# Kernel tuning notes

Hardware: AMD Instinct MI355X
Metric: run time of the kernel (lower is better)

The kernel has to match this reference:

```python
import jax, jax.numpy as jnp
import numpy as np

B, H, W = 16, 1024, 1024
EPS = 1e-7
FG_PROB = 0.1  # foreground pixel probability for synthetic gt


def setup_inputs() -> dict:
    key = jax.random.key(0)
    k1, k2 = jax.random.split(key)
    probs = jax.random.normal(k1, (B, 2, H, W), dtype=jnp.float32)
    gt = (jax.random.uniform(k2, (B, H, W)) < FG_PROB).astype(jnp.float32)
    gt_f_num = gt.sum(axis=(1, 2))  # per-sample foreground pixel count (float)
    return {"probs": probs, "gt": gt, "gt_f_num": gt_f_num, "img_h": H, "img_w": W}


def reference(probs, gt, gt_f_num, img_h, img_w):
    # foreground probability, clamped
    pc = jax.nn.softmax(probs, axis=1)[:, 1, :, :]
    pc = jnp.clip(pc, EPS, 1.0 - EPS)
    b = pc.shape[0]
    f_loss = -(gt * jnp.log(pc)).reshape(b, -1)          # [B, N]
    b_loss = -((1.0 - gt) * jnp.log(1.0 - pc)).reshape(b, -1)  # [B, N]
    n = b_loss.shape[1]

    # sort background loss descending per sample; top gt_f_num[i] entries are
    # "difficult" negatives, the rest are "simple" (equivalent to the torch
    # gather-into-zero-buffers since only sums/counts are taken afterwards)
    sorted_b = -jnp.sort(-b_loss, axis=1)                # descending, [B, N]
    k = gt_f_num.astype(jnp.int32)                       # int(gt_f_num[i])
    mask = jnp.arange(n, dtype=jnp.int32)[None, :] < k[:, None]  # [B, N]

    difficult_sum = jnp.sum(jnp.where(mask, sorted_b, 0.0), axis=1)
    simple_sum = jnp.sum(jnp.where(mask, 0.0, sorted_b), axis=1)
    difficult_num = jnp.sum(mask & (sorted_b != 0.0), axis=1).astype(jnp.float32)

    difficult_b_loss = difficult_sum / (difficult_num + 1e-16)
    simple_b_loss = simple_sum / (float(img_h * img_w) + 1e-16)
    f_loss_mean = f_loss.sum(axis=1) / (gt_f_num + 1e-16)

    return difficult_b_loss.mean() + f_loss_mean.mean() + simple_b_loss.mean()
```

## Files before the change

kernel.cpp:

```cpp
#include <hip/hip_runtime.h>
#include <math.h>

#define NB 16
#define NPIX 1048576
#define BINS 2048
#define CHUNKS 64
#define TPB_A 1024
#define PIX_PER_BLOCK (NPIX / CHUNKS)
#define QUADS 4
#define REPL 8
#define TPB_B 256
#define BINS_PER_CHUNK (BINS / TPB_B)
#define BLOSS_MAX 16.7f
#define BINW (BLOSS_MAX / (float)BINS)
#define B_CAP 16.636f
#define F_CAP 16.1181f

__device__ __forceinline__ void fadd_glb(float* p, float v) {
    __hip_atomic_fetch_add(p, v, __ATOMIC_RELAXED, __HIP_MEMORY_SCOPE_AGENT);
}

__global__ __launch_bounds__(TPB_A, 8) void pass_a(
    const float* __restrict__ probs, const float* __restrict__ gt,
    unsigned* __restrict__ g_cnt, float* __restrict__ f_sum,
    float* __restrict__ b_sum)
{
    __shared__ unsigned s_cnt[BINS];
    __shared__ float s_redf[TPB_A / 64];
    __shared__ float s_redb[TPB_A / 64];

    const int tid = threadIdx.x;
    #pragma unroll
    for (int j = 0; j < BINS / TPB_A; ++j) s_cnt[j * TPB_A + tid] = 0u;
    __syncthreads();

    const int blk = blockIdx.x;
    const int b = blk / CHUNKS;
    const int chunk = blk % CHUNKS;
    const float* p0 = probs + (size_t)b * 2 * NPIX;
    const float* p1 = p0 + NPIX;
    const float* gp = gt + (size_t)b * NPIX;
    const int base = chunk * PIX_PER_BLOCK;
    const float scale = (float)BINS / BLOSS_MAX;

    float4 A0[QUADS], A1[QUADS], G[QUADS];
    #pragma unroll
    for (int q = 0; q < QUADS; ++q) {
        const int i = base + ((q * TPB_A + tid) << 2);
        A0[q] = *(const float4*)(p0 + i);
        A1[q] = *(const float4*)(p1 + i);
        G[q]  = *(const float4*)(gp + i);
    }

    float f_acc = 0.f, b_acc = 0.f;
    #pragma unroll
    for (int q = 0; q < QUADS; ++q) {
        const float dv[4] = {A1[q].x - A0[q].x, A1[q].y - A0[q].y,
                             A1[q].z - A0[q].z, A1[q].w - A0[q].w};
        const float gv[4] = {G[q].x, G[q].y, G[q].z, G[q].w};
        #pragma unroll
        for (int c = 0; c < 4; ++c) {
            const float d = dv[c];
            const float g = gv[c];
            const float sp = fmaxf(d, 0.f) + __logf(1.f + __expf(-fabsf(d)));
            f_acc += g * fminf(sp - d, F_CAP);
            const float bl = fminf(sp, B_CAP);
            b_acc += (1.f - g) * bl;
            if (g < 0.5f) {
                int bin = (int)(bl * scale);
                bin = bin < (BINS - 1) ? bin : (BINS - 1);
                atomicAdd(&s_cnt[bin], 1u);
            }
        }
    }
    __syncthreads();

    {
        unsigned* dst = g_cnt + ((size_t)b * REPL + (chunk & (REPL - 1))) * BINS;
        #pragma unroll
        for (int j = 0; j < BINS / TPB_A; ++j) {
            const int bin = j * TPB_A + tid;
            const unsigned c = s_cnt[bin];
            if (c) atomicAdd(&dst[bin], c);
        }
    }

    #pragma unroll
    for (int o = 32; o > 0; o >>= 1) {
        f_acc += __shfl_down(f_acc, o, 64);
        b_acc += __shfl_down(b_acc, o, 64);
    }
    if ((tid & 63) == 0) { s_redf[tid >> 6] = f_acc; s_redb[tid >> 6] = b_acc; }
    __syncthreads();
    if (tid == 0) {
        float f = 0.f, bs = 0.f;
        #pragma unroll
        for (int w = 0; w < TPB_A / 64; ++w) { f += s_redf[w]; bs += s_redb[w]; }
        fadd_glb(&f_sum[b], f);
        fadd_glb(&b_sum[b], bs);
    }
}

__global__ __launch_bounds__(TPB_B) void pass_b(
    const unsigned* __restrict__ g_cnt, const float* __restrict__ f_sum,
    const float* __restrict__ b_sum, const float* __restrict__ gt_f_num,
    float* __restrict__ terms)
{
    __shared__ unsigned s_cnt[BINS];
    __shared__ unsigned s_suf[TPB_B];
    __shared__ double s_wsuf[TPB_B];
    __shared__ double s_dsum;

    const int b = blockIdx.x;
    const int t = threadIdx.x;

    #pragma unroll
    for (int j = 0; j < BINS_PER_CHUNK; ++j) {
        const int bin = j * TPB_B + t;
        unsigned c = 0;
        #pragma unroll
        for (int r = 0; r < REPL; ++r)
            c += g_cnt[((size_t)b * REPL + r) * BINS + bin];
        s_cnt[bin] = c;
    }
    __syncthreads();

    unsigned c = 0; double w = 0.0;
    const int cb = t * BINS_PER_CHUNK;
    #pragma unroll
    for (int j = 0; j < BINS_PER_CHUNK; ++j) {
        const unsigned cc = s_cnt[cb + j];
        c += cc;
        w += (double)cc * (double)(((float)(cb + j) + 0.5f) * BINW);
    }
    s_suf[t] = c; s_wsuf[t] = w;
    __syncthreads();

    for (int off = 1; off < TPB_B; off <<= 1) {
        const unsigned ac = (t + off < TPB_B) ? s_suf[t + off] : 0u;
        const double aw = (t + off < TPB_B) ? s_wsuf[t + off] : 0.0;
        __syncthreads();
        s_suf[t] += ac; s_wsuf[t] += aw;
        __syncthreads();
    }

    const long long kk = (long long)gt_f_num[b];
    const unsigned long long n_pos = (unsigned long long)s_suf[0];
    const unsigned long long suf_me = s_suf[t];
    const unsigned long long suf_nx = (t + 1 < TPB_B) ? s_suf[t + 1] : 0ull;

    if (kk > 0 && (unsigned long long)kk < n_pos &&
        suf_nx < (unsigned long long)kk && (unsigned long long)kk <= suf_me) {
        unsigned long long cum = suf_nx;
        double W = (t + 1 < TPB_B) ? s_wsuf[t + 1] : 0.0;
        int bstar = cb;
        for (int j = BINS_PER_CHUNK - 1; j >= 0; --j) {
            const int bin = cb + j;
            const unsigned cc = s_cnt[bin];
            if (cum + cc >= (unsigned long long)kk) { bstar = bin; break; }
            cum += cc;
            W += (double)cc * (double)(((float)bin + 0.5f) * BINW);
        }
        const double partial = (double)(kk - (long long)cum);
        s_dsum = W + partial * (double)(((float)bstar + 0.5f) * BINW);
    }
    __syncthreads();

    if (t == 0) {
        const double S_total = (double)b_sum[b];
        const double fs = (double)f_sum[b];
        const double gfn = (double)gt_f_num[b];
        double dsum, dnum;
        if (kk <= 0) { dsum = 0.0; dnum = 0.0; }
        else if ((unsigned long long)kk >= n_pos) { dsum = S_total; dnum = (double)n_pos; }
        else { dsum = s_dsum; dnum = (double)kk; }
        const double term = dsum / (dnum + 1e-16)
                          + fs / (gfn + 1e-16)
                          + (S_total - dsum) / ((double)NPIX + 1e-16);
        terms[b] = (float)term;
    }
}

__global__ void pass_c(const float* __restrict__ terms, float* __restrict__ out)
{
    if (threadIdx.x == 0 && blockIdx.x == 0) {
        float s = 0.f;
        #pragma unroll
        for (int i = 0; i < NB; ++i) s += terms[i];
        out[0] = s / (float)NB;
    }
}

extern "C" void kernel_launch(void* const* d_in, const int* in_sizes, int n_in,
                              void* d_out, int out_size, void* d_ws, size_t ws_size,
                              hipStream_t stream) {
    const float* probs = (const float*)d_in[0];
    const float* gt    = (const float*)d_in[1];
    const float* gfn   = (const float*)d_in[2];
    char* ws = (char*)d_ws;

    const size_t hist_bytes = (size_t)NB * REPL * BINS * 4;
    unsigned* g_cnt = (unsigned*)ws;
    float*    f_sum = (float*)(ws + hist_bytes);
    float*    b_sum = f_sum + NB;
    float*    terms = b_sum + NB;

    hipMemsetAsync(ws, 0, hist_bytes + 2 * NB * sizeof(float), stream);

    hipLaunchKernelGGL(pass_a, dim3(NB * CHUNKS), dim3(TPB_A), 0, stream,
                       probs, gt, g_cnt, f_sum, b_sum);
    hipLaunchKernelGGL(pass_b, dim3(NB), dim3(TPB_B), 0, stream,
                       g_cnt, f_sum, b_sum, gfn, terms);
    hipLaunchKernelGGL(pass_c, dim3(1), dim3(64), 0, stream,
                       terms, (float*)d_out);
}
```

Baseline: 250.7 us.

## Stream pass_a inputs through double-buffered LDS tiles via global_load_lds

Pass A no longer loads all of a thread's pixels into registers up front. Each block now walks its chunk in 1024-pixel tiles, staging probs and gt into double-buffered shared memory with asynchronous global-to-LDS loads, and prefetches the next tile while computing the current one. The grid changes to 2048 blocks of 256 threads. The goal is to overlap memory latency with the softmax, log and histogram work and to lower register pressure. The cost is a block-wide barrier on every tile and about 24 KB of extra LDS per block, which may limit occupancy. Correctness also depends on the compiler waiting for the LDS DMA to finish before the data is read.

After: 249.7 us. Within noise of the previous version (-0.4%).

```diff
diff --git a/kernel.cpp b/kernel.cpp
--- a/kernel.cpp
+++ b/kernel.cpp
@@ -4,10 +4,11 @@
 #define NB 16
 #define NPIX 1048576
 #define BINS 2048
-#define CHUNKS 64
-#define TPB_A 1024
+#define CHUNKS 128
+#define TPB_A 256
 #define PIX_PER_BLOCK (NPIX / CHUNKS)
-#define QUADS 4
+#define TILE_PX 1024
+#define NT (PIX_PER_BLOCK / TILE_PX)
 #define REPL 8
 #define TPB_B 256
 #define BINS_PER_CHUNK (BINS / TPB_B)
@@ -20,19 +21,27 @@
     __hip_atomic_fetch_add(p, v, __ATOMIC_RELAXED, __HIP_MEMORY_SCOPE_AGENT);
 }
 
-__global__ __launch_bounds__(TPB_A, 8) void pass_a(
+__device__ __forceinline__ void gl_lds16(const float* g, float* lds) {
+    __builtin_amdgcn_global_load_lds(
+        (const __attribute__((address_space(1))) unsigned*)g,
+        (__attribute__((address_space(3))) unsigned*)lds, 16, 0, 0);
+}
+
+__global__ __launch_bounds__(TPB_A) void pass_a(
     const float* __restrict__ probs, const float* __restrict__ gt,
     unsigned* __restrict__ g_cnt, float* __restrict__ f_sum,
     float* __restrict__ b_sum)
 {
     __shared__ unsigned s_cnt[BINS];
+    __shared__ float s_p0[2][TILE_PX];
+    __shared__ float s_p1[2][TILE_PX];
+    __shared__ float s_g [2][TILE_PX];
     __shared__ float s_redf[TPB_A / 64];
     __shared__ float s_redb[TPB_A / 64];
 
     const int tid = threadIdx.x;
     #pragma unroll
     for (int j = 0; j < BINS / TPB_A; ++j) s_cnt[j * TPB_A + tid] = 0u;
-    __syncthreads();
 
     const int blk = blockIdx.x;
     const int b = blk / CHUNKS;
@@ -43,21 +52,24 @@
     const int base = chunk * PIX_PER_BLOCK;
     const float scale = (float)BINS / BLOSS_MAX;
 
-    float4 A0[QUADS], A1[QUADS], G[QUADS];
-    #pragma unroll
-    for (int q = 0; q < QUADS; ++q) {
-        const int i = base + ((q * TPB_A + tid) << 2);
-        A0[q] = *(const float4*)(p0 + i);
-        A1[q] = *(const float4*)(p1 + i);
-        G[q]  = *(const float4*)(gp + i);
-    }
+    auto issue = [&](int t, int buf) {
+        const int off = base + t * TILE_PX + (tid << 2);
+        gl_lds16(p0 + off, &s_p0[buf][tid << 2]);
+        gl_lds16(p1 + off, &s_p1[buf][tid << 2]);
+        gl_lds16(gp + off, &s_g [buf][tid << 2]);
+    };
 
     float f_acc = 0.f, b_acc = 0.f;
-    #pragma unroll
-    for (int q = 0; q < QUADS; ++q) {
-        const float dv[4] = {A1[q].x - A0[q].x, A1[q].y - A0[q].y,
-                             A1[q].z - A0[q].z, A1[q].w - A0[q].w};
-        const float gv[4] = {G[q].x, G[q].y, G[q].z, G[q].w};
+    issue(0, 0);
+    for (int t = 0; t < NT; ++t) {
+        __syncthreads();
+        if (t + 1 < NT) issue(t + 1, (t + 1) & 1);
+        const int buf = t & 1;
+        const float4 v0 = *(const float4*)&s_p0[buf][tid << 2];
+        const float4 v1 = *(const float4*)&s_p1[buf][tid << 2];
+        const float4 vg = *(const float4*)&s_g [buf][tid << 2];
+        const float dv[4] = {v1.x - v0.x, v1.y - v0.y, v1.z - v0.z, v1.w - v0.w};
+        const float gv[4] = {vg.x, vg.y, vg.z, vg.w};
         #pragma unroll
         for (int c = 0; c < 4; ++c) {
             const float d = dv[c];
```
